# Kernel tuning notes

Hardware: AMD Instinct MI355X
Metric: run time of the kernel (lower is better)

The kernel has to match this reference:

```python
import jax, jax.numpy as jnp
import numpy as np

LN_EPS = 1e-5


def setup_inputs() -> dict:
    key = jax.random.key(0)
    ks = jax.random.split(key, 11)
    B, C, H, W, F = 32, 256, 128, 128, 256  # in_planes=C, features=F
    s = lambda k, shape: (jax.random.normal(k, shape, jnp.float32) * 0.05)
    return {
        "x": jax.random.normal(ks[0], (B, C, H, W), jnp.float32),
        # ContextBlock.conv_mask: Conv2d(C, 1, 1)
        "mask_w": s(ks[1], (1, C, 1, 1)),
        "mask_b": s(ks[2], (1,)),
        # channel_mul_conv: Conv2d(C,C,1) -> LayerNorm([C,1,1]) -> ReLU -> Conv2d(C,C,1)
        "cm1_w": s(ks[3], (C, C, 1, 1)),
        "cm1_b": s(ks[4], (C,)),
        "ln_g": jnp.ones((C,), jnp.float32),
        "ln_b": jnp.zeros((C,), jnp.float32),
        "cm2_w": s(ks[5], (C, C, 1, 1)),
        "cm2_b": s(ks[6], (C,)),
        # output_conv: Conv2d(C, F, 5, stride=1, padding=2, groups=1)
        "out_w": s(ks[7], (F, C, 5, 5)),
        "out_b": s(ks[8], (F,)),
        # att: Linear(C, F)
        "att_w": s(ks[9], (F, C)),
        "att_b": s(ks[10], (F,)),
    }


def reference(x, mask_w, mask_b, cm1_w, cm1_b, ln_g, ln_b, cm2_w, cm2_b,
              out_w, out_b, att_w, att_b):
    B, C, H, W = x.shape
    xf = x.reshape(B, C, H * W)
    # --- ContextBlock.spatial_pool ('att') ---
    logits = jnp.einsum('bcn,c->bn', xf, mask_w[0, :, 0, 0]) + mask_b[0]  # (B, HW)
    attn = jax.nn.softmax(logits, axis=-1)
    context = jnp.einsum('bcn,bn->bc', xf, attn)  # (B, C) global context
    # --- channel_mul_conv chain on (B, C, 1, 1) ---
    h = jnp.einsum('oc,bc->bo', cm1_w[:, :, 0, 0], context) + cm1_b
    mu = jnp.mean(h, axis=-1, keepdims=True)
    var = jnp.var(h, axis=-1, keepdims=True)  # LayerNorm over [C,1,1]
    h = (h - mu) * jax.lax.rsqrt(var + LN_EPS) * ln_g + ln_b
    h = jax.nn.relu(h)
    h = jnp.einsum('oc,bc->bo', cm2_w[:, :, 0, 0], h) + cm2_b
    input_x = jax.nn.sigmoid(h)  # ContextBlock output (channel_mul term), (B, C)
    # --- output_conv: 5x5 conv, pad=2 on 1x1 spatial -> only center tap contributes ---
    out = jnp.einsum('bc,fc->bf', input_x, out_w[:, :, 2, 2]) + out_b  # (B, F)
    # --- att gate ---
    att = jax.nn.sigmoid(input_x @ att_w.T + att_b)  # (B, F)
    return (att * out)[:, :, None, None]  # (B, F, 1, 1)
```

## Files before the change

kernel.cpp:

```cpp
#include <hip/hip_runtime.h>

typedef unsigned int uint;

#define BATCH 32
#define NCH   256
#define HW    16384

__global__ __launch_bounds__(256, 4) void spool_kernel(
    const float* __restrict__ x, const float* __restrict__ mask_w,
    const float* __restrict__ mask_b, float* __restrict__ ctxnum,
    float* __restrict__ zbuf)
{
    __shared__ float wlds[NCH];
    __shared__ float wpart[4][64];
    __shared__ float earr[64];

    const int tid  = threadIdx.x;
    const int b    = blockIdx.x >> 6;
    const int blk  = blockIdx.x & 63;
    const int r    = tid >> 3;
    const int m    = tid & 7;
    const int wave = tid >> 6;
    const int rl   = r & 7;

    wlds[tid] = mask_w[tid];
    const float mb = mask_b[0];
    __syncthreads();

    float wc[8];
    #pragma unroll
    for (int it = 0; it < 8; ++it) wc[it] = wlds[(it << 5) + r];

    float acc[8] = {0.f,0.f,0.f,0.f,0.f,0.f,0.f,0.f};
    float zacc = 0.f;

    const float* xb = x + ((size_t)b << 22) + ((size_t)r << 14) + (m << 3);

    for (int g = 0; g < 4; ++g) {
        const int n0 = (blk << 8) + (g << 6);

        float4 d0[8], d1[8];
        float la[8] = {0.f,0.f,0.f,0.f,0.f,0.f,0.f,0.f};
        #pragma unroll
        for (int it = 0; it < 8; ++it) {
            const float4* p = (const float4*)(xb + ((size_t)it << 19) + n0);
            d0[it] = p[0];
            d1[it] = p[1];
            const float w = wc[it];
            la[0] += w * d0[it].x; la[1] += w * d0[it].y;
            la[2] += w * d0[it].z; la[3] += w * d0[it].w;
            la[4] += w * d1[it].x; la[5] += w * d1[it].y;
            la[6] += w * d1[it].z; la[7] += w * d1[it].w;
        }
        #pragma unroll
        for (int k = 0; k < 8; ++k) {
            float v = la[k];
            v += __shfl_xor(v, 8, 64);
            v += __shfl_xor(v, 16, 64);
            v += __shfl_xor(v, 32, 64);
            la[k] = v;
        }
        if (rl == 0) {
            float4* wp = (float4*)&wpart[wave][m << 3];
            wp[0] = make_float4(la[0], la[1], la[2], la[3]);
            wp[1] = make_float4(la[4], la[5], la[6], la[7]);
        }
        __syncthreads();

        if (tid < 64) {
            const float l = wpart[0][tid] + wpart[1][tid]
                          + wpart[2][tid] + wpart[3][tid] + mb;
            const float e = expf(l);
            earr[tid] = e;
            zacc += e;
        }
        __syncthreads();

        float el[8];
        #pragma unroll
        for (int j = 0; j < 8; ++j) el[j] = earr[(m << 3) + j];
        #pragma unroll
        for (int it = 0; it < 8; ++it) {
            acc[it] += d0[it].x * el[0] + d0[it].y * el[1]
                     + d0[it].z * el[2] + d0[it].w * el[3]
                     + d1[it].x * el[4] + d1[it].y * el[5]
                     + d1[it].z * el[6] + d1[it].w * el[7];
        }
    }

    float ctxv = 0.f;
    #pragma unroll
    for (int it = 0; it < 8; ++it) {
        float v = acc[it];
        v += __shfl_xor(v, 1, 64);
        v += __shfl_xor(v, 2, 64);
        v += __shfl_xor(v, 4, 64);
        if (m == it) ctxv = v;
    }
    atomicAdd(&ctxnum[(b << 8) + (m << 5) + r], ctxv);

    if (tid < 64) {
        float s = zacc;
        #pragma unroll
        for (int off = 32; off > 0; off >>= 1) s += __shfl_down(s, off, 64);
        if (tid == 0) atomicAdd(&zbuf[b], s);
    }
}

__global__ __launch_bounds__(256) void tail_kernel(
    const float* __restrict__ ctxnum, const float* __restrict__ zbuf,
    const float* __restrict__ cm1_w, const float* __restrict__ cm1_b,
    const float* __restrict__ ln_g,  const float* __restrict__ ln_b,
    const float* __restrict__ cm2_w, const float* __restrict__ cm2_b,
    const float* __restrict__ out_w, const float* __restrict__ out_b,
    const float* __restrict__ att_w, const float* __restrict__ att_b,
    float* __restrict__ outp)
{
    const int b = blockIdx.x, t = threadIdx.x;
    __shared__ float v[NCH];
    __shared__ float red[8];

    const float zinv = 1.f / zbuf[b];
    v[t] = ctxnum[(b << 8) + t] * zinv;
    __syncthreads();

    float h = cm1_b[t];
    {
        const float4* wr = (const float4*)(cm1_w + ((size_t)t << 8));
        #pragma unroll
        for (int jj = 0; jj < 64; ++jj) {
            const float4 w = wr[jj];
            const int c = jj << 2;
            h += w.x * v[c] + w.y * v[c + 1] + w.z * v[c + 2] + w.w * v[c + 3];
        }
    }

    float s1 = h, s2 = h * h;
    #pragma unroll
    for (int off = 32; off > 0; off >>= 1) {
        s1 += __shfl_down(s1, off, 64);
        s2 += __shfl_down(s2, off, 64);
    }
    if ((t & 63) == 0) { red[t >> 6] = s1; red[4 + (t >> 6)] = s2; }
    __syncthreads();
    const float mu  = (red[0] + red[1] + red[2] + red[3]) * (1.f / 256.f);
    const float ex2 = (red[4] + red[5] + red[6] + red[7]) * (1.f / 256.f);
    const float rs  = rsqrtf(ex2 - mu * mu + 1e-5f);
    float sv = (h - mu) * rs * ln_g[t] + ln_b[t];
    sv = fmaxf(sv, 0.f);
    __syncthreads();
    v[t] = sv;
    __syncthreads();

    float h2 = cm2_b[t];
    {
        const float4* wr = (const float4*)(cm2_w + ((size_t)t << 8));
        #pragma unroll
        for (int jj = 0; jj < 64; ++jj) {
            const float4 w = wr[jj];
            const int c = jj << 2;
            h2 += w.x * v[c] + w.y * v[c + 1] + w.z * v[c + 2] + w.w * v[c + 3];
        }
    }
    const float ix = 1.f / (1.f + expf(-h2));
    __syncthreads();
    v[t] = ix;
    __syncthreads();

    float o = out_b[t];
    {
        const float* ow = out_w + (size_t)t * 6400 + 12;
        #pragma unroll 8
        for (int c = 0; c < 256; ++c) o += ow[c * 25] * v[c];
    }

    float a = att_b[t];
    {
        const float4* wr = (const float4*)(att_w + ((size_t)t << 8));
        #pragma unroll
        for (int jj = 0; jj < 64; ++jj) {
            const float4 w = wr[jj];
            const int c = jj << 2;
            a += w.x * v[c] + w.y * v[c + 1] + w.z * v[c + 2] + w.w * v[c + 3];
        }
    }
    a = 1.f / (1.f + expf(-a));

    outp[(b << 8) + t] = a * o;
}

extern "C" void kernel_launch(void* const* d_in, const int* in_sizes, int n_in,
                              void* d_out, int out_size, void* d_ws, size_t ws_size,
                              hipStream_t stream) {
    (void)in_sizes; (void)n_in; (void)out_size; (void)ws_size;
    const float* x      = (const float*)d_in[0];
    const float* mask_w = (const float*)d_in[1];
    const float* mask_b = (const float*)d_in[2];
    const float* cm1_w  = (const float*)d_in[3];
    const float* cm1_b  = (const float*)d_in[4];
    const float* ln_g   = (const float*)d_in[5];
    const float* ln_b   = (const float*)d_in[6];
    const float* cm2_w  = (const float*)d_in[7];
    const float* cm2_b  = (const float*)d_in[8];
    const float* out_w  = (const float*)d_in[9];
    const float* out_b  = (const float*)d_in[10];
    const float* att_w  = (const float*)d_in[11];
    const float* att_b  = (const float*)d_in[12];

    float* zbuf   = (float*)d_ws;
    float* ctxnum = zbuf + 32;

    hipMemsetAsync(d_ws, 0, (32 + BATCH * NCH) * sizeof(float), stream);

    spool_kernel<<<BATCH * 64, 256, 0, stream>>>(x, mask_w, mask_b, ctxnum, zbuf);

    tail_kernel<<<BATCH, 256, 0, stream>>>(ctxnum, zbuf,
                                           cm1_w, cm1_b, ln_g, ln_b,
                                           cm2_w, cm2_b, out_w, out_b,
                                           att_w, att_b, (float*)d_out);
}
```

Baseline: 920.3 us.

## Give each wave its own 16-pixel slice to remove per-group block barriers

Work is repartitioned so each wave owns a distinct 16-pixel slice of every 64-pixel group. The mask logits can then be reduced entirely with in-wave shuffles, and each wave computes its own exp values. This removes the two __syncthreads per group and the shared-memory logit staging. The cost is redundant exp computation across lanes (the zacc sum is scaled by 1/16 to compensate), more registers (16 float4 per thread), and relaxed launch bounds that may reduce occupancy on a memory-bound streaming kernel.

```diff
diff --git a/kernel.cpp b/kernel.cpp
--- a/kernel.cpp
+++ b/kernel.cpp
@@ -6,105 +6,96 @@
 #define NCH   256
 #define HW    16384
 
-__global__ __launch_bounds__(256, 4) void spool_kernel(
+__global__ __launch_bounds__(256) void spool_kernel(
     const float* __restrict__ x, const float* __restrict__ mask_w,
     const float* __restrict__ mask_b, float* __restrict__ ctxnum,
     float* __restrict__ zbuf)
 {
     __shared__ float wlds[NCH];
-    __shared__ float wpart[4][64];
-    __shared__ float earr[64];
+    __shared__ float wpart[4][NCH];
+    __shared__ float zarr[4];
 
     const int tid  = threadIdx.x;
     const int b    = blockIdx.x >> 6;
     const int blk  = blockIdx.x & 63;
-    const int r    = tid >> 3;
-    const int m    = tid & 7;
     const int wave = tid >> 6;
-    const int rl   = r & 7;
+    const int l    = tid & 63;
+    const int q    = l & 3;
+    const int rr   = l >> 2;
 
     wlds[tid] = mask_w[tid];
     const float mb = mask_b[0];
     __syncthreads();
 
-    float wc[8];
-    #pragma unroll
-    for (int it = 0; it < 8; ++it) wc[it] = wlds[(it << 5) + r];
-
-    float acc[8] = {0.f,0.f,0.f,0.f,0.f,0.f,0.f,0.f};
+    float wcr[16];
+    #pragma unroll
+    for (int i = 0; i < 16; ++i) wcr[i] = wlds[(i << 4) + rr];
+
+    float acc[16];
+    #pragma unroll
+    for (int i = 0; i < 16; ++i) acc[i] = 0.f;
     float zacc = 0.f;
 
-    const float* xb = x + ((size_t)b << 22) + ((size_t)r << 14) + (m << 3);
+    const float* xb = x + ((size_t)b << 22) + ((size_t)rr << 14)
+                        + (wave << 4) + (q << 2);
 
     for (int g = 0; g < 4; ++g) {
         const int n0 = (blk << 8) + (g << 6);
 
-        float4 d0[8], d1[8];
-        float la[8] = {0.f,0.f,0.f,0.f,0.f,0.f,0.f,0.f};
-        #pragma unroll
-        for (int it = 0; it < 8; ++it) {
-            const float4* p = (const float4*)(xb + ((size_t)it << 19) + n0);
-            d0[it] = p[0];
-            d1[it] = p[1];
-            const float w = wc[it];
-            la[0] += w * d0[it].x; la[1] += w * d0[it].y;
-            la[2] += w * d0[it].z; la[3] += w * d0[it].w;
-            la[4] += w * d1[it].x; la[5] += w * d1[it].y;
-            la[6] += w * d1[it].z; la[7] += w * d1[it].w;
-        }
-        #pragma unroll
-        for (int k = 0; k < 8; ++k) {
+        float4 d[16];
+        float la[4] = {0.f, 0.f, 0.f, 0.f};
+        #pragma unroll
+        for (int i = 0; i < 16; ++i) {
+            d[i] = *(const float4*)(xb + ((size_t)i << 18) + n0);
+            const float w = wcr[i];
+            la[0] += w * d[i].x; la[1] += w * d[i].y;
+            la[2] += w * d[i].z; la[3] += w * d[i].w;
+        }
+
+        #pragma unroll
+        for (int k = 0; k < 4; ++k) {
             float v = la[k];
+            v += __shfl_xor(v, 4, 64);
             v += __shfl_xor(v, 8, 64);
             v += __shfl_xor(v, 16, 64);
             v += __shfl_xor(v, 32, 64);
             la[k] = v;
         }
-        if (rl == 0) {
-            float4* wp = (float4*)&wpart[wave][m << 3];
-            wp[0] = make_float4(la[0], la[1], la[2], la[3]);
-            wp[1] = make_float4(la[4], la[5], la[6], la[7]);
-        }
-        __syncthreads();
-
-        if (tid < 64) {
-            const float l = wpart[0][tid] + wpart[1][tid]
-                          + wpart[2][tid] + wpart[3][tid] + mb;
-            const float e = expf(l);
-            earr[tid] = e;
-            zacc += e;
-        }
-        __syncthreads();
-
-        float el[8];
-        #pragma unroll
-        for (int j = 0; j < 8; ++j) el[j] = earr[(m << 3) + j];
-        #pragma unroll
-        for (int it = 0; it < 8; ++it) {
-            acc[it] += d0[it].x * el[0] + d0[it].y * el[1]
-                     + d0[it].z * el[2] + d0[it].w * el[3]
-                     + d1[it].x * el[4] + d1[it].y * el[5]
-                     + d1[it].z * el[6] + d1[it].w * el[7];
-        }
-    }
-
-    float ctxv = 0.f;
-    #pragma unroll
-    for (int it = 0; it < 8; ++it) {
-        float v = acc[it];
+
+        float e[4];
+        #pragma unroll
+        for (int k = 0; k < 4; ++k) e[k] = expf(la[k] + mb);
+        zacc += e[0] + e[1] + e[2] + e[3];
+        #pragma unroll
+        for (int i = 0; i < 16; ++i) {
+            acc[i] += d[i].x * e[0] + d[i].y * e[1]
+                    + d[i].z * e[2] + d[i].w * e[3];
+        }
+    }
+
+    #pragma unroll
+    for (int i = 0; i < 16; ++i) {
+        float v = acc[i];
         v += __shfl_xor(v, 1, 64);
         v += __shfl_xor(v, 2, 64);
-        v += __shfl_xor(v, 4, 64);
-        if (m == it) ctxv = v;
-    }
-    atomicAdd(&ctxnum[(b << 8) + (m << 5) + r], ctxv);
-
-    if (tid < 64) {
+        acc[i] = v;
+    }
+    if (q == 0) {
+        #pragma unroll
+        for (int i = 0; i < 16; ++i) wpart[wave][(i << 4) + rr] = acc[i];
+    }
+    {
         float s = zacc;
         #pragma unroll
         for (int off = 32; off > 0; off >>= 1) s += __shfl_down(s, off, 64);
-        if (tid == 0) atomicAdd(&zbuf[b], s);
-    }
+        if (l == 0) zarr[wave] = s * (1.f / 16.f);
+    }
+    __syncthreads();
+
+    const float ctxv = wpart[0][tid] + wpart[1][tid]
+                     + wpart[2][tid] + wpart[3][tid];
+    atomicAdd(&ctxnum[(b << 8) + tid], ctxv);
+    if (tid == 0) atomicAdd(&zbuf[b], zarr[0] + zarr[1] + zarr[2] + zarr[3]);
 }
 
 __global__ __launch_bounds__(256) void tail_kernel(
```

Measured after the change: 792.7 us. 13.9% less time.
